# Optimization experiments

Measured on AMD Instinct MI355X. Metric: run time of the kernel, lower is better.

Reference implementation:

```python
import math
import jax, jax.numpy as jnp
import numpy as np

N_HEAD = 16

def skew(QEr):
    # QEr: (B, H, L, L) where last dim indexes relative positions via Er_t
    B, H, L, _ = QEr.shape
    padded = jnp.pad(QEr, ((0, 0), (0, 0), (0, 0), (1, 0)))        # (B,H,L,L+1)
    reshaped = padded.reshape(B, H, L + 1, L)                       # (B,H,L+1,L)
    return reshaped[:, :, 1:, :]                                    # (B,H,L,L)

def setup_inputs() -> dict:
    key = jax.random.key(0)
    ks = jax.random.split(key, 6)
    B, L, D = 2, 2048, 1024
    hs = D // N_HEAD
    block_size = 2048
    return {
        "x": jax.random.normal(ks[0], (B, L, D), dtype=jnp.float32),
        "W_attn": jax.random.normal(ks[1], (D, 3 * D), dtype=jnp.float32) * 0.02,
        "b_attn": jnp.zeros((3 * D,), dtype=jnp.float32),
        "W_proj": jax.random.normal(ks[2], (D, D), dtype=jnp.float32) * 0.02,
        "b_proj": jnp.zeros((D,), dtype=jnp.float32),
        "Er": jax.random.normal(ks[3], (block_size, hs), dtype=jnp.float32),
    }

def reference(x, W_attn, b_attn, W_proj, b_proj, Er):
    B, L, D = x.shape
    H = N_HEAD
    hs = D // H
    qkv = x @ W_attn + b_attn                                       # (B,L,3D)
    q, k, v = jnp.split(qkv, 3, axis=-1)
    q = q.reshape(B, L, H, hs).transpose(0, 2, 1, 3)                # (B,H,L,hs)
    k = k.reshape(B, L, H, hs).transpose(0, 2, 1, 3)
    v = v.reshape(B, L, H, hs).transpose(0, 2, 1, 3)
    start = Er.shape[0] - L
    Er_t = Er[start:, :].T                                          # (hs,L)
    QEr = jnp.einsum('bhld,de->bhle', q, Er_t)                      # (B,H,L,L)
    Srel = skew(QEr)
    QK_t = jnp.einsum('bhqd,bhkd->bhqk', q, k)
    scale = 1.0 / math.sqrt(hs)
    att = (QK_t + Srel) * scale
    causal = jnp.tril(jnp.ones((L, L), dtype=bool))
    att = jnp.where(causal[None, None, :, :], att, -jnp.inf)
    att = jax.nn.softmax(att, axis=-1)
    y = jnp.einsum('bhqk,bhkd->bhqd', att, v)                       # (B,H,L,hs)
    y = y.transpose(0, 2, 1, 3).reshape(B, L, D)
    return y @ W_proj + b_proj
```

## Files before the change

### kernel.cpp

```cpp
#include <hip/hip_runtime.h>
#include <stdint.h>

#define L_SEQ 2048
#define D_MODEL 1024
#define NHEAD 16
#define HS 64
#define B_BATCH 2
#define QSCALE 0.1803368801111243f

typedef __bf16 bf16x8 __attribute__((ext_vector_type(8)));
typedef float f32x4 __attribute__((ext_vector_type(4)));

__device__ __forceinline__ float fexp2(float x) {
  return __builtin_amdgcn_exp2f(x);
}

__device__ __forceinline__ unsigned short f2b(float f) {
  unsigned int u = __float_as_uint(f);
  u += 0x7fffu + ((u >> 16) & 1u);
  return (unsigned short)(u >> 16);
}
__device__ __forceinline__ unsigned int pk2(float a, float b) {
  return (unsigned int)f2b(a) | ((unsigned int)f2b(b) << 16);
}
__device__ __forceinline__ unsigned int cvtpk(float a, float b) {
  unsigned int r;
  asm("v_cvt_pk_bf16_f32 %0, %1, %2" : "=v"(r) : "v"(a), "v"(b));
  return r;
}

union U8 { uint4 v; unsigned short s[8]; };

__device__ __forceinline__ void ldsload16(const unsigned short* g, unsigned short* l) {
  __builtin_amdgcn_global_load_lds(
      (const __attribute__((address_space(1))) unsigned int*)g,
      (__attribute__((address_space(3))) unsigned int*)l, 16, 0, 0);
}

__device__ __forceinline__ bf16x8 frag_ld(const unsigned short* base, int row, int ks, int quad) {
  const int unit = (ks * 4 + quad) ^ (row & 7);
  return *(const bf16x8*)(base + row * 64 + unit * 8);
}

__global__ __launch_bounds__(256) void prep(
    const float* __restrict__ x, const float* __restrict__ Wa,
    const float* __restrict__ Wp, const float* __restrict__ Er,
    unsigned short* __restrict__ xb, unsigned short* __restrict__ wabT,
    unsigned short* __restrict__ wpbT, unsigned short* __restrict__ erb) {
  __shared__ unsigned short tt[64][65];
  int gb = blockIdx.x;
  if (gb < 2048) {
    int i = gb * 256 + threadIdx.x;
    const float4* s4 = (const float4*)x;
    float4 a = s4[i * 2], b = s4[i * 2 + 1];
    U8 u;
    u.s[0] = f2b(a.x); u.s[1] = f2b(a.y); u.s[2] = f2b(a.z); u.s[3] = f2b(a.w);
    u.s[4] = f2b(b.x); u.s[5] = f2b(b.y); u.s[6] = f2b(b.z); u.s[7] = f2b(b.w);
    ((uint4*)xb)[i] = u.v;
    return;
  }
  gb -= 2048;
  if (gb < 68) {
    int i = gb * 256 + threadIdx.x;
    if (i < 16384) {
      const float4* s4 = (const float4*)Er;
      float4 a = s4[i * 2], b = s4[i * 2 + 1];
      U8 u;
      u.s[0] = f2b(a.x); u.s[1] = f2b(a.y); u.s[2] = f2b(a.z); u.s[3] = f2b(a.w);
      u.s[4] = f2b(b.x); u.s[5] = f2b(b.y); u.s[6] = f2b(b.z); u.s[7] = f2b(b.w);
      ((uint4*)erb)[i] = u.v;
    } else {
      ((uint4*)erb)[i] = make_uint4(0u, 0u, 0u, 0u);
    }
    return;
  }
  gb -= 68;
  const float* src;
  unsigned short* dst;
  int N, nbx;
  if (gb < 768) { src = Wa; dst = wabT; N = 3072; nbx = 48; }
  else { gb -= 768; src = Wp; dst = wpbT; N = 1024; nbx = 16; }
  const int n0 = (gb % nbx) * 64, k0 = (gb / nbx) * 64;
  const int c = threadIdx.x & 63, r0 = threadIdx.x >> 6;
#pragma unroll
  for (int i = 0; i < 16; i++) {
    int r = r0 * 16 + i;
    tt[r][c] = f2b(src[(size_t)(k0 + r) * N + n0 + c]);
  }
  __syncthreads();
  const int n = threadIdx.x >> 2, ks = (threadIdx.x & 3) * 16;
  U8 u0, u1;
#pragma unroll
  for (int j = 0; j < 8; j++) {
    u0.s[j] = tt[ks + j][n];
    u1.s[j] = tt[ks + 8 + j][n];
  }
  unsigned short* d = dst + (size_t)(n0 + n) * 1024 + k0 + ks;
  *(uint4*)d = u0.v;
  *(uint4*)(d + 8) = u1.v;
}

__global__ __launch_bounds__(256, 3) void gemm_qkv(
    const unsigned short* __restrict__ A, const unsigned short* __restrict__ Bt,
    const float* __restrict__ bias, unsigned short* __restrict__ qbuf,
    unsigned short* __restrict__ kbuf, unsigned short* __restrict__ vbufT,
    int M, int N, int K) {
  __shared__ unsigned short As[128 * 64];
  __shared__ unsigned short Bs[128 * 64];
  const int tid = threadIdx.x, lane = tid & 63, w = tid >> 6;
  const int wm = w >> 1, wn = w & 1, quad = lane >> 4, lc = lane & 15;
  const int wgid = blockIdx.x;
  const int xcd = wgid & 7, t = wgid >> 3;
  const int bnr = t % 3, bm = t / 3;
  const int bn = xcd * 3 + bnr;
  const int l8 = lane >> 3, u8 = ((lane & 7) ^ l8) * 8;
  const unsigned short* Ab = A + (size_t)bm * 128 * K;
  const unsigned short* Bb = Bt + (size_t)bn * 128 * K;

  f32x4 z4 = {0.f, 0.f, 0.f, 0.f};
  f32x4 acc[4][4];
#pragma unroll
  for (int mb = 0; mb < 4; mb++)
#pragma unroll
    for (int nb = 0; nb < 4; nb++) acc[mb][nb] = z4;

  for (int kk = 0; kk < K; kk += 64) {
    if (kk) __syncthreads();
#pragma unroll
    for (int i = 0; i < 4; i++) {
      int ch = w * 4 + i;
      ldsload16(Ab + (size_t)(ch * 8 + l8) * K + kk + u8, &As[ch * 512]);
      ldsload16(Bb + (size_t)(ch * 8 + l8) * K + kk + u8, &Bs[ch * 512]);
    }
    __syncthreads();
#pragma unroll
    for (int ks = 0; ks < 2; ks++) {
      bf16x8 af[4], bfv[4];
#pragma unroll
      for (int mb = 0; mb < 4; mb++) af[mb] = frag_ld(As, wm * 64 + mb * 16 + lc, ks, quad);
#pragma unroll
      for (int nb = 0; nb < 4; nb++) bfv[nb] = frag_ld(Bs, wn * 64 + nb * 16 + lc, ks, quad);
#pragma unroll
      for (int mb = 0; mb < 4; mb++)
#pragma unroll
        for (int nb = 0; nb < 4; nb++)
          acc[mb][nb] = __builtin_amdgcn_mfma_f32_16x16x32_bf16(af[mb], bfv[nb],
                                                               acc[mb][nb], 0, 0, 0);
    }
  }

#pragma unroll
  for (int nb = 0; nb < 4; nb++) {
    const int n = bn * 128 + wn * 64 + nb * 16 + lc;
    const float bv = bias[n];
    const int which = n >> 10;
    const int rem = n & 1023;
    const int h = rem >> 6, d = rem & 63;
#pragma unroll
    for (int mb = 0; mb < 4; mb++) {
      const int m0 = bm * 128 + wm * 64 + mb * 16 + quad * 4;
      const int b = m0 >> 11, l0 = m0 & 2047;
      if (which == 2) {
        float v0 = acc[mb][nb][0] + bv, v1 = acc[mb][nb][1] + bv;
        float v2 = acc[mb][nb][2] + bv, v3 = acc[mb][nb][3] + bv;
        uint2 pv;
        pv.x = pk2(v0, v1);
        pv.y = pk2(v2, v3);
        *(uint2*)&vbufT[((size_t)(b * NHEAD + h) * HS + d) * L_SEQ + l0] = pv;
      } else {
        const float sc = which == 0 ? QSCALE : 1.0f;
        unsigned short* dst = (which == 0) ? qbuf : kbuf;
#pragma unroll
        for (int reg = 0; reg < 4; reg++) {
          float val = (acc[mb][nb][reg] + bv) * sc;
          dst[((size_t)(b * NHEAD + h) * L_SEQ + l0 + reg) * HS + d] = f2b(val);
        }
      }
    }
  }
}

__global__ __launch_bounds__(256, 3) void gemm_proj(
    const unsigned short* __restrict__ A, const unsigned short* __restrict__ Bt,
    const float* __restrict__ bias, float* __restrict__ out, int M, int N, int K) {
  __shared__ unsigned short As[128 * 64];
  __shared__ unsigned short Bs[64 * 64];
  const int tid = threadIdx.x, lane = tid & 63, w = tid >> 6;
  const int quad = lane >> 4, lc = lane & 15;
  const int wgid = blockIdx.x;
  const int xcd = wgid & 7, t = wgid >> 3;
  const int bnr = t & 1, bm = t >> 1;
  const int bn = xcd * 2 + bnr;
  const int l8 = lane >> 3, u8 = ((lane & 7) ^ l8) * 8;
  const unsigned short* Ab = A + (size_t)bm * 128 * K;
  const unsigned short* Bb = Bt + (size_t)bn * 64 * K;

  f32x4 z4 = {0.f, 0.f, 0.f, 0.f};
  f32x4 acc[2][4];
#pragma unroll
  for (int mb = 0; mb < 2; mb++)
#pragma unroll
    for (int nb = 0; nb < 4; nb++) acc[mb][nb] = z4;

  for (int kk = 0; kk < K; kk += 64) {
    if (kk) __syncthreads();
#pragma unroll
    for (int i = 0; i < 4; i++) {
      int ch = w * 4 + i;
      ldsload16(Ab + (size_t)(ch * 8 + l8) * K + kk + u8, &As[ch * 512]);
    }
#pragma unroll
    for (int i = 0; i < 2; i++) {
      int ch = w * 2 + i;
      ldsload16(Bb + (size_t)(ch * 8 + l8) * K + kk + u8, &Bs[ch * 512]);
    }
    __syncthreads();
#pragma unroll
    for (int ks = 0; ks < 2; ks++) {
      bf16x8 af[2], bfv[4];
#pragma unroll
      for (int mb = 0; mb < 2; mb++) af[mb] = frag_ld(As, w * 32 + mb * 16 + lc, ks, quad);
#pragma unroll
      for (int nb = 0; nb < 4; nb++) bfv[nb] = frag_ld(Bs, nb * 16 + lc, ks, quad);
#pragma unroll
      for (int mb = 0; mb < 2; mb++)
#pragma unroll
        for (int nb = 0; nb < 4; nb++)
          acc[mb][nb] = __builtin_amdgcn_mfma_f32_16x16x32_bf16(af[mb], bfv[nb],
                                                               acc[mb][nb], 0, 0, 0);
    }
  }

#pragma unroll
  for (int nb = 0; nb < 4; nb++) {
    const int n = bn * 64 + nb * 16 + lc;
    const float bv = bias[n];
#pragma unroll
    for (int mb = 0; mb < 2; mb++) {
#pragma unroll
      for (int reg = 0; reg < 4; reg++) {
        const int m = bm * 128 + w * 32 + mb * 16 + quad * 4 + reg;
        out[(size_t)m * N + n] = acc[mb][nb][reg] + bv;
      }
    }
  }
}

__global__ __launch_bounds__(256, 3) void flash_attn_rel(
    const unsigned short* __restrict__ qb, const unsigned short* __restrict__ kb,
    const unsigned short* __restrict__ vbT, const unsigned short* __restrict__ erb,
    unsigned short* __restrict__ yb) {
  __shared__ unsigned short Ks[64 * 64];
  __shared__ unsigned short Vt[64 * 64];
  __shared__ unsigned short Es[128 * 64];
  __shared__ float Twf[4][16 * 84];

  const int tid = threadIdx.x, lane = tid & 63, w = tid >> 6;
  const int quad = lane >> 4, lc = lane & 15;
  const int wgid = blockIdx.x;
  const int xcd = wgid & 7, r7 = wgid >> 3;
  const int bhr = r7 & 3, y = r7 >> 2;
  const int bh = xcd * 4 + bhr;
  const int b = bh >> 4, h = bh & 15;
  const int qt = 31 - y;
  const int q0 = qt * 64;
  const int qg0 = q0 + w * 16;
  const size_t hoff = (size_t)bh * L_SEQ * HS;
  float* TwfW = Twf[w];
  unsigned short* TwpW = (unsigned short*)TwfW;
  const int l8 = lane >> 3, u8 = ((lane & 7) ^ l8) * 8;
  const f32x4 z4 = {0.f, 0.f, 0.f, 0.f};

  bf16x8 qf[2];
  {
    const unsigned short* qrow = qb + hoff + (size_t)(qg0 + lc) * HS;
    qf[0] = *(const bf16x8*)(qrow + quad * 8);
    qf[1] = *(const bf16x8*)(qrow + 32 + quad * 8);
  }
  f32x4 Oacc[4];
#pragma unroll
  for (int db = 0; db < 4; db++) Oacc[db] = z4;
  float psum_acc = 0.0f;

  const unsigned short* kgb = kb + hoff;
  const unsigned short* vgbT = vbT + (size_t)bh * HS * L_SEQ;
  const int ebw = 48 - w * 16;
  const int e_anchor = (L_SEQ - 64) - q0;

  for (int k0 = 0; k0 <= q0; k0 += 64) {
    __syncthreads();
#pragma unroll
    for (int i = 0; i < 2; i++) {
      int ch = w * 2 + i;
      ldsload16(kgb + (size_t)(k0 + ch * 8 + l8) * HS + u8, &Ks[ch * 512]);
      ldsload16(vgbT + (size_t)(ch * 8 + l8) * L_SEQ + k0 + u8, &Vt[ch * 512]);
    }
    if (k0 == 0) {
#pragma unroll
      for (int i = 0; i < 4; i++) {
        int ch = w * 4 + i;
        ldsload16(erb + (size_t)(e_anchor + ch * 8 + l8) * HS + u8, &Es[ch * 512]);
      }
    } else {
#pragma unroll
      for (int i = 0; i < 2; i++) {
        int ch = w * 2 + i;
        const int er = k0 + 64 + ch * 8;
        ldsload16(erb + (size_t)(e_anchor + er + l8) * HS + u8,
                  &Es[(er & 127) * 64]);
      }
    }
    __syncthreads();

    f32x4 sacc[4], tacc[5];
#pragma unroll
    for (int i = 0; i < 4; i++) sacc[i] = z4;
#pragma unroll
    for (int i = 0; i < 5; i++) tacc[i] = z4;
    const int eb0 = k0 + ebw;
#pragma unroll
    for (int ks = 0; ks < 2; ks++) {
#pragma unroll
      for (int kbi = 0; kbi < 4; kbi++) {
        bf16x8 a = frag_ld(Ks, kbi * 16 + lc, ks, quad);
        sacc[kbi] = __builtin_amdgcn_mfma_f32_16x16x32_bf16(a, qf[ks], sacc[kbi], 0, 0, 0);
      }
#pragma unroll
      for (int eb = 0; eb < 5; eb++) {
        bf16x8 a = frag_ld(Es, (eb0 + eb * 16 + lc) & 127, ks, quad);
        tacc[eb] = __builtin_amdgcn_mfma_f32_16x16x32_bf16(a, qf[ks], tacc[eb], 0, 0, 0);
      }
    }
#pragma unroll
    for (int eb = 0; eb < 5; eb++)
      *(f32x4*)&TwfW[lc * 84 + eb * 16 + quad * 4] = tacc[eb];
    asm volatile("" ::: "memory");

    float p[4][4], ps = 0.0f;
    const int tbase = lc * 84 + (15 - lc);
    if (k0 == q0) {
      const int qrow = w * 16 + lc;
#pragma unroll
      for (int kbi = 0; kbi < 4; kbi++)
#pragma unroll
        for (int reg = 0; reg < 4; reg++) {
          const int kk = kbi * 16 + quad * 4 + reg;
          float t = TwfW[tbase + kk];
          float v = (kk > qrow) ? -1e30f : (sacc[kbi][reg] + t);
          p[kbi][reg] = fexp2(v);
          ps += p[kbi][reg];
        }
    } else {
#pragma unroll
      for (int kbi = 0; kbi < 4; kbi++)
#pragma unroll
        for (int reg = 0; reg < 4; reg++) {
          float t = TwfW[tbase + kbi * 16 + quad * 4 + reg];
          p[kbi][reg] = fexp2(sacc[kbi][reg] + t);
          ps += p[kbi][reg];
        }
    }
    psum_acc += ps;
#pragma unroll
    for (int kbi = 0; kbi < 4; kbi++) {
      uint2 pk;
      pk.x = cvtpk(p[kbi][0], p[kbi][1]);
      pk.y = cvtpk(p[kbi][2], p[kbi][3]);
      const int k = kbi * 16 + quad * 4;
      *(uint2*)&TwpW[lc * 64 + (((k >> 3) ^ (lc & 7)) << 3) + (k & 7)] = pk;
    }
    asm volatile("" ::: "memory");

#pragma unroll
    for (int ks = 0; ks < 2; ks++) {
      bf16x8 pf = frag_ld(TwpW, lc, ks, quad);
#pragma unroll
      for (int db = 0; db < 4; db++) {
        bf16x8 av = frag_ld(Vt, db * 16 + lc, ks, quad);
        Oacc[db] = __builtin_amdgcn_mfma_f32_16x16x32_bf16(av, pf, Oacc[db], 0, 0, 0);
      }
    }
  }

  psum_acc += __shfl_xor(psum_acc, 16, 64);
  psum_acc += __shfl_xor(psum_acc, 32, 64);
  const float inv = 1.0f / psum_acc;

  __syncthreads();
  unsigned short* Yt = Es;
#pragma unroll
  for (int db = 0; db < 4; db++) {
    uint2 pk;
    pk.x = cvtpk(Oacc[db][0] * inv, Oacc[db][1] * inv);
    pk.y = cvtpk(Oacc[db][2] * inv, Oacc[db][3] * inv);
    *(uint2*)&Yt[(w * 16 + lc) * 72 + db * 16 + quad * 4] = pk;
  }
  __syncthreads();
  {
    const int r = tid >> 2, seg = (tid & 3) * 16;
    uint4 a0 = *(const uint4*)&Yt[r * 72 + seg];
    uint4 a1 = *(const uint4*)&Yt[r * 72 + seg + 8];
    unsigned short* d = yb + (size_t)((size_t)b * L_SEQ + q0 + r) * D_MODEL + h * HS + seg;
    *(uint4*)d = a0;
    *(uint4*)(d + 8) = a1;
  }
}

extern "C" void kernel_launch(void* const* d_in, const int* in_sizes, int n_in,
                              void* d_out, int out_size, void* d_ws, size_t ws_size,
                              hipStream_t stream) {
  const float* x = (const float*)d_in[0];
  const float* W_attn = (const float*)d_in[1];
  const float* b_attn = (const float*)d_in[2];
  const float* W_proj = (const float*)d_in[3];
  const float* b_proj = (const float*)d_in[4];
  const float* Er = (const float*)d_in[5];
  float* out = (float*)d_out;

  const int n_x = B_BATCH * L_SEQ * D_MODEL;
  const int n_wa = D_MODEL * 3 * D_MODEL;
  const int n_wp = D_MODEL * D_MODEL;
  const int n_er_pad = (L_SEQ + 128) * HS;
  const int n_head = B_BATCH * NHEAD * L_SEQ * HS;

  unsigned short* xb = (unsigned short*)d_ws;
  unsigned short* wabT = xb + n_x;
  unsigned short* wpbT = wabT + n_wa;
  unsigned short* erb = wpbT + n_wp;
  unsigned short* qbuf = erb + n_er_pad;
  unsigned short* kbuf = qbuf + n_head;
  unsigned short* vbufT = kbuf + n_head;
  unsigned short* ybuf = vbufT + n_head;

  prep<<<3140, 256, 0, stream>>>(x, W_attn, W_proj, Er, xb, wabT, wpbT, erb);

  gemm_qkv<<<768, 256, 0, stream>>>(xb, wabT, b_attn, qbuf, kbuf, vbufT,
                                    B_BATCH * L_SEQ, 3 * D_MODEL, D_MODEL);

  flash_attn_rel<<<1024, 256, 0, stream>>>(qbuf, kbuf, vbufT, erb, ybuf);

  gemm_proj<<<512, 256, 0, stream>>>(ybuf, wpbT, b_proj, out,
                                     B_BATCH * L_SEQ, D_MODEL, D_MODEL);
}
```

Measured before the change: 190.3 us.

## Retile QKV GEMM to 256x192 with double-buffered LDS prefetch

Rewrites the QKV projection GEMM to use 512-thread blocks computing 256x192 output tiles, giving 256 workgroups in place of 768. The next K-slice is prefetched into a second LDS buffer while MFMAs run on the current one, which removes one barrier per iteration and overlaps global loads with compute. MFMA sections are wrapped in s_setprio. The cost is 112KB of dynamic shared memory per block, more accumulator registers, and fewer waves per CU.

After: 198.0 us. 1.04x slower.

```diff
diff --git a/kernel.cpp b/kernel.cpp
--- a/kernel.cpp
+++ b/kernel.cpp
@@ -100,69 +100,101 @@
   *(uint4*)(d + 8) = u1.v;
 }
 
-__global__ __launch_bounds__(256, 3) void gemm_qkv(
+__global__ __launch_bounds__(512, 2) void gemm_qkv(
     const unsigned short* __restrict__ A, const unsigned short* __restrict__ Bt,
     const float* __restrict__ bias, unsigned short* __restrict__ qbuf,
     unsigned short* __restrict__ kbuf, unsigned short* __restrict__ vbufT,
     int M, int N, int K) {
-  __shared__ unsigned short As[128 * 64];
-  __shared__ unsigned short Bs[128 * 64];
+  extern __shared__ unsigned short SH[];
   const int tid = threadIdx.x, lane = tid & 63, w = tid >> 6;
-  const int wm = w >> 1, wn = w & 1, quad = lane >> 4, lc = lane & 15;
+  const int wm = w >> 2, wn = w & 3, quad = lane >> 4, lc = lane & 15;
   const int wgid = blockIdx.x;
   const int xcd = wgid & 7, t = wgid >> 3;
-  const int bnr = t % 3, bm = t / 3;
-  const int bn = xcd * 3 + bnr;
+  const int bn = xcd * 2 + (t & 1);
+  const int bm = t >> 1;
   const int l8 = lane >> 3, u8 = ((lane & 7) ^ l8) * 8;
-  const unsigned short* Ab = A + (size_t)bm * 128 * K;
-  const unsigned short* Bb = Bt + (size_t)bn * 128 * K;
+  const unsigned short* Agb = A + (size_t)bm * 256 * K;
+  const unsigned short* Bgb = Bt + (size_t)bn * 192 * K;
 
   f32x4 z4 = {0.f, 0.f, 0.f, 0.f};
-  f32x4 acc[4][4];
-#pragma unroll
-  for (int mb = 0; mb < 4; mb++)
-#pragma unroll
-    for (int nb = 0; nb < 4; nb++) acc[mb][nb] = z4;
-
-  for (int kk = 0; kk < K; kk += 64) {
-    if (kk) __syncthreads();
-#pragma unroll
-    for (int i = 0; i < 4; i++) {
-      int ch = w * 4 + i;
-      ldsload16(Ab + (size_t)(ch * 8 + l8) * K + kk + u8, &As[ch * 512]);
-      ldsload16(Bb + (size_t)(ch * 8 + l8) * K + kk + u8, &Bs[ch * 512]);
+  f32x4 acc[8][3];
+#pragma unroll
+  for (int mf = 0; mf < 8; mf++)
+#pragma unroll
+    for (int j = 0; j < 3; j++) acc[mf][j] = z4;
+
+#pragma unroll
+  for (int i = 0; i < 4; i++) {
+    int ch = w * 4 + i;
+    ldsload16(Agb + (size_t)(ch * 8 + l8) * K + u8, SH + ch * 512);
+  }
+#pragma unroll
+  for (int i = 0; i < 3; i++) {
+    int ch = w * 3 + i;
+    ldsload16(Bgb + (size_t)(ch * 8 + l8) * K + u8, SH + 16384 + ch * 512);
+  }
+  __syncthreads();
+
+  const int nkt = K >> 6;
+  for (int kt = 0; kt < nkt; kt++) {
+    unsigned short* Abuf = SH + (kt & 1) * 28672;
+    unsigned short* Bbuf = Abuf + 16384;
+    unsigned short* Anx = SH + ((kt + 1) & 1) * 28672;
+    unsigned short* Bnx = Anx + 16384;
+    const int kkn = (kt + 1) << 6;
+    const bool pre = (kt + 1) < nkt;
+    bf16x8 bf[3][2];
+#pragma unroll
+    for (int p = 0; p < 4; p++) {
+      if (p == 0) {
+#pragma unroll
+        for (int j = 0; j < 3; j++)
+#pragma unroll
+          for (int ks = 0; ks < 2; ks++)
+            bf[j][ks] = frag_ld(Bbuf, wn * 48 + j * 16 + lc, ks, quad);
+      }
+      bf16x8 af[2][2];
+#pragma unroll
+      for (int i = 0; i < 2; i++)
+#pragma unroll
+        for (int ks = 0; ks < 2; ks++)
+          af[i][ks] = frag_ld(Abuf, wm * 128 + (p * 2 + i) * 16 + lc, ks, quad);
+      if (pre) {
+        int ch = w * 4 + p;
+        ldsload16(Agb + (size_t)(ch * 8 + l8) * K + kkn + u8, Anx + ch * 512);
+        if (p < 3) {
+          int chb = w * 3 + p;
+          ldsload16(Bgb + (size_t)(chb * 8 + l8) * K + kkn + u8, Bnx + chb * 512);
+        }
+      }
+      __builtin_amdgcn_s_setprio(1);
+#pragma unroll
+      for (int ks = 0; ks < 2; ks++)
+#pragma unroll
+        for (int i = 0; i < 2; i++)
+#pragma unroll
+          for (int j = 0; j < 3; j++)
+            acc[p * 2 + i][j] = __builtin_amdgcn_mfma_f32_16x16x32_bf16(
+                af[i][ks], bf[j][ks], acc[p * 2 + i][j], 0, 0, 0);
+      __builtin_amdgcn_s_setprio(0);
     }
     __syncthreads();
-#pragma unroll
-    for (int ks = 0; ks < 2; ks++) {
-      bf16x8 af[4], bfv[4];
-#pragma unroll
-      for (int mb = 0; mb < 4; mb++) af[mb] = frag_ld(As, wm * 64 + mb * 16 + lc, ks, quad);
-#pragma unroll
-      for (int nb = 0; nb < 4; nb++) bfv[nb] = frag_ld(Bs, wn * 64 + nb * 16 + lc, ks, quad);
-#pragma unroll
-      for (int mb = 0; mb < 4; mb++)
-#pragma unroll
-        for (int nb = 0; nb < 4; nb++)
-          acc[mb][nb] = __builtin_amdgcn_mfma_f32_16x16x32_bf16(af[mb], bfv[nb],
-                                                               acc[mb][nb], 0, 0, 0);
-    }
-  }
-
-#pragma unroll
-  for (int nb = 0; nb < 4; nb++) {
-    const int n = bn * 128 + wn * 64 + nb * 16 + lc;
+  }
+
+#pragma unroll
+  for (int j = 0; j < 3; j++) {
+    const int n = bn * 192 + wn * 48 + j * 16 + lc;
     const float bv = bias[n];
     const int which = n >> 10;
     const int rem = n & 1023;
     const int h = rem >> 6, d = rem & 63;
 #pragma unroll
-    for (int mb = 0; mb < 4; mb++) {
-      const int m0 = bm * 128 + wm * 64 + mb * 16 + quad * 4;
+    for (int mf = 0; mf < 8; mf++) {
+      const int m0 = bm * 256 + wm * 128 + mf * 16 + quad * 4;
       const int b = m0 >> 11, l0 = m0 & 2047;
       if (which == 2) {
-        float v0 = acc[mb][nb][0] + bv, v1 = acc[mb][nb][1] + bv;
-        float v2 = acc[mb][nb][2] + bv, v3 = acc[mb][nb][3] + bv;
+        float v0 = acc[mf][j][0] + bv, v1 = acc[mf][j][1] + bv;
+        float v2 = acc[mf][j][2] + bv, v3 = acc[mf][j][3] + bv;
         uint2 pv;
         pv.x = pk2(v0, v1);
         pv.y = pk2(v2, v3);
@@ -172,7 +204,7 @@
         unsigned short* dst = (which == 0) ? qbuf : kbuf;
 #pragma unroll
         for (int reg = 0; reg < 4; reg++) {
-          float val = (acc[mb][nb][reg] + bv) * sc;
+          float val = (acc[mf][j][reg] + bv) * sc;
           dst[((size_t)(b * NHEAD + h) * L_SEQ + l0 + reg) * HS + d] = f2b(val);
         }
       }
@@ -434,8 +466,8 @@
 
   prep<<<3140, 256, 0, stream>>>(x, W_attn, W_proj, Er, xb, wabT, wpbT, erb);
 
-  gemm_qkv<<<768, 256, 0, stream>>>(xb, wabT, b_attn, qbuf, kbuf, vbufT,
-                                    B_BATCH * L_SEQ, 3 * D_MODEL, D_MODEL);
+  gemm_qkv<<<256, 512, 114688, stream>>>(xb, wabT, b_attn, qbuf, kbuf, vbufT,
+                                         B_BATCH * L_SEQ, 3 * D_MODEL, D_MODEL);
 
   flash_attn_rel<<<1024, 256, 0, stream>>>(qbuf, kbuf, vbufT, erb, ybuf);
 
```
